# Kernel tuning notes

Measured on AMD Instinct MI355X. Metric: run time of the kernel, lower is better.

## Reference

```python
import jax, jax.numpy as jnp
import numpy as np

REPARAM_OFFSET = 2.0 ** -18
PEDESTAL = REPARAM_OFFSET ** 2            # 2**-36
BETA_MIN = 1e-6
BOUND_BETA = float(np.sqrt(BETA_MIN + PEDESTAL))
BOUND_A = float(np.sqrt(0.0 + PEDESTAL))


def nn_reparam(p, bound):
    # NonNegativeParametrizer.forward: lower_bound(p, bound)**2 - pedestal
    return jnp.maximum(p, bound) ** 2 - PEDESTAL


def setup_inputs() -> dict:
    key = jax.random.key(0)
    kx, ka = jax.random.split(key)
    C, R = 192, 8
    x = jax.random.normal(kx, (8, C, 256, 256), dtype=jnp.float32)
    # parameters stored in reparam-init space: init(v) = sqrt(max(v + ped, ped))
    beta = jnp.sqrt(jnp.ones((C,), jnp.float32) + PEDESTAL)
    A = jnp.sqrt(0.1 * jax.random.uniform(ka, (C, R), dtype=jnp.float32) + PEDESTAL)
    return {"x": x, "beta": beta, "A": A}


def reference(x, beta, A):
    beta_r = nn_reparam(beta, BOUND_BETA)[None, :, None, None]   # [1,C,1,1]
    A_r = nn_reparam(A, BOUND_A)                                  # [C,r]
    x2 = x * x
    T = jnp.einsum('nchw,cr->nrhw', x2, A_r)                      # low-rank projection
    denom_sq = jnp.einsum('cr,nrhw->nchw', A_r, T) + beta_r
    return x * jax.lax.rsqrt(denom_sq)                            # inverse=False -> rsqrt
```

## Files before the change

kernel.cpp:

```cpp
#include <hip/hip_runtime.h>


#define N_IMG 8
#define C_CH 192
#define R_RK 8
#define HW 65536
#define PXB 128
#define CSLICES 8
#define CPT (C_CH / CSLICES)
#define NTHR 512
#define BLOCKS_PER_IMG (HW / PXB)

#define PEDESTAL_F 1.4551915228366852e-11f
#define BOUND_A_F 3.814697265625e-06f
#define BOUND_BETA_F 1.0000072759311364e-03f

typedef float v2 __attribute__((ext_vector_type(2)));

__global__ __launch_bounds__(NTHR, 8) void lrgdn_kernel(
    const float* __restrict__ x,
    const float* __restrict__ beta,
    const float* __restrict__ A,
    float* __restrict__ out)
{
    __shared__ float sA[C_CH][R_RK];
    __shared__ float sB[C_CH];
    __shared__ v2 sT[CSLICES][R_RK][64];

    const int tid = threadIdx.x;

    for (int i = tid; i < C_CH * R_RK; i += NTHR) {
        float a = fmaxf(A[i], BOUND_A_F);
        sA[i >> 3][i & 7] = a * a - PEDESTAL_F;
    }
    if (tid < C_CH) {
        float b = fmaxf(beta[tid], BOUND_BETA_F);
        sB[tid] = b * b - PEDESTAL_F;
    }
    __syncthreads();

    const int blk  = blockIdx.x;
    const int n    = blk / BLOCKS_PER_IMG;
    const int p0   = (blk % BLOCKS_PER_IMG) * PXB;
    const int lane = tid & 63;
    const int cs   = tid >> 6;
    const int c0   = cs * CPT;

    const float* xn = x   + (size_t)n * (C_CH * HW) + p0 + (size_t)c0 * HW + 2 * lane;
    float*       on = out + (size_t)n * (C_CH * HW) + p0 + (size_t)c0 * HW + 2 * lane;

    v2 T[R_RK];
#pragma unroll
    for (int r = 0; r < R_RK; ++r) T[r] = (v2)0.f;

#pragma unroll 8
    for (int i = 0; i < CPT; ++i) {
        v2 v = *reinterpret_cast<const v2*>(xn + (size_t)i * HW);
        v2 s = v * v;
#pragma unroll
        for (int r = 0; r < R_RK; ++r) {
            T[r] += s * sA[c0 + i][r];
        }
    }

#pragma unroll
    for (int r = 0; r < R_RK; ++r) {
        sT[cs][r][lane] = T[r];
    }
    __syncthreads();

#pragma unroll
    for (int r = 0; r < R_RK; ++r) {
        v2 a01 = sT[0][r][lane] + sT[1][r][lane];
        v2 a23 = sT[2][r][lane] + sT[3][r][lane];
        v2 a45 = sT[4][r][lane] + sT[5][r][lane];
        v2 a67 = sT[6][r][lane] + sT[7][r][lane];
        T[r] = (a01 + a23) + (a45 + a67);
    }

#pragma unroll 8
    for (int i = 0; i < CPT; ++i) {
        int c = c0 + i;
        v2 v = *reinterpret_cast<const v2*>(xn + (size_t)i * HW);
        v2 d;
        d.x = sB[c];
        d.y = d.x;
#pragma unroll
        for (int r = 0; r < R_RK; ++r) {
            d += sA[c][r] * T[r];
        }
        v2 o;
        o.x = v.x * __builtin_amdgcn_rsqf(d.x);
        o.y = v.y * __builtin_amdgcn_rsqf(d.y);
        __builtin_nontemporal_store(o, reinterpret_cast<v2*>(on + (size_t)i * HW));
    }
}

extern "C" void kernel_launch(void* const* d_in, const int* in_sizes, int n_in,
                              void* d_out, int out_size, void* d_ws, size_t ws_size,
                              hipStream_t stream) {
    const float* x    = (const float*)d_in[0];
    const float* beta = (const float*)d_in[1];
    const float* A    = (const float*)d_in[2];
    float* out = (float*)d_out;

    dim3 grid(N_IMG * BLOCKS_PER_IMG);
    dim3 block(NTHR);
    hipLaunchKernelGGL(lrgdn_kernel, grid, block, 0, stream, x, beta, A, out);
}
```

Baseline: 206.2 us.

## Cache x in registers, halve pixel tile, and remap blocks across XCDs

Each thread now loads its 24 channel values once into registers with nontemporal loads and reuses them for the output pass, so the second global read of x goes away. The pixel tile drops from 128 to 64 with scalar per-thread access instead of float2, which doubles the grid. A block-index permutation spreads consecutive work across the 8 XCDs. The cost is more register pressure, narrower memory transactions and more blocks, each repeating the setup of the A and beta tables.

```diff
diff --git a/kernel.cpp b/kernel.cpp
--- a/kernel.cpp
+++ b/kernel.cpp
@@ -5,17 +5,16 @@
 #define C_CH 192
 #define R_RK 8
 #define HW 65536
-#define PXB 128
+#define PXB 64
 #define CSLICES 8
 #define CPT (C_CH / CSLICES)
 #define NTHR 512
 #define BLOCKS_PER_IMG (HW / PXB)
+#define NBLK (N_IMG * BLOCKS_PER_IMG)
 
 #define PEDESTAL_F 1.4551915228366852e-11f
 #define BOUND_A_F 3.814697265625e-06f
 #define BOUND_BETA_F 1.0000072759311364e-03f
-
-typedef float v2 __attribute__((ext_vector_type(2)));
 
 __global__ __launch_bounds__(NTHR, 8) void lrgdn_kernel(
     const float* __restrict__ x,
@@ -25,7 +24,7 @@
 {
     __shared__ float sA[C_CH][R_RK];
     __shared__ float sB[C_CH];
-    __shared__ v2 sT[CSLICES][R_RK][64];
+    __shared__ float sT[CSLICES][R_RK][64];
 
     const int tid = threadIdx.x;
 
@@ -39,27 +38,33 @@
     }
     __syncthreads();
 
-    const int blk  = blockIdx.x;
-    const int n    = blk / BLOCKS_PER_IMG;
-    const int p0   = (blk % BLOCKS_PER_IMG) * PXB;
+    const int b = blockIdx.x;
+    const int w = (b & 7) * (NBLK / 8) + (b >> 3);
+    const int n    = w / BLOCKS_PER_IMG;
+    const int p0   = (w % BLOCKS_PER_IMG) * PXB;
     const int lane = tid & 63;
     const int cs   = tid >> 6;
     const int c0   = cs * CPT;
 
-    const float* xn = x   + (size_t)n * (C_CH * HW) + p0 + (size_t)c0 * HW + 2 * lane;
-    float*       on = out + (size_t)n * (C_CH * HW) + p0 + (size_t)c0 * HW + 2 * lane;
+    const float* xn = x   + (size_t)n * (C_CH * HW) + p0 + (size_t)c0 * HW + lane;
+    float*       on = out + (size_t)n * (C_CH * HW) + p0 + (size_t)c0 * HW + lane;
 
-    v2 T[R_RK];
+    float xr[CPT];
 #pragma unroll
-    for (int r = 0; r < R_RK; ++r) T[r] = (v2)0.f;
+    for (int i = 0; i < CPT; ++i) {
+        xr[i] = __builtin_nontemporal_load(xn + (size_t)i * HW);
+    }
 
-#pragma unroll 8
+    float T[R_RK];
+#pragma unroll
+    for (int r = 0; r < R_RK; ++r) T[r] = 0.f;
+
+#pragma unroll
     for (int i = 0; i < CPT; ++i) {
-        v2 v = *reinterpret_cast<const v2*>(xn + (size_t)i * HW);
-        v2 s = v * v;
+        float s = xr[i] * xr[i];
 #pragma unroll
         for (int r = 0; r < R_RK; ++r) {
-            T[r] += s * sA[c0 + i][r];
+            T[r] = fmaf(s, sA[c0 + i][r], T[r]);
         }
     }
 
@@ -71,28 +76,23 @@
 
 #pragma unroll
     for (int r = 0; r < R_RK; ++r) {
-        v2 a01 = sT[0][r][lane] + sT[1][r][lane];
-        v2 a23 = sT[2][r][lane] + sT[3][r][lane];
-        v2 a45 = sT[4][r][lane] + sT[5][r][lane];
-        v2 a67 = sT[6][r][lane] + sT[7][r][lane];
+        float a01 = sT[0][r][lane] + sT[1][r][lane];
+        float a23 = sT[2][r][lane] + sT[3][r][lane];
+        float a45 = sT[4][r][lane] + sT[5][r][lane];
+        float a67 = sT[6][r][lane] + sT[7][r][lane];
         T[r] = (a01 + a23) + (a45 + a67);
     }
 
-#pragma unroll 8
+#pragma unroll
     for (int i = 0; i < CPT; ++i) {
         int c = c0 + i;
-        v2 v = *reinterpret_cast<const v2*>(xn + (size_t)i * HW);
-        v2 d;
-        d.x = sB[c];
-        d.y = d.x;
+        float d = sB[c];
 #pragma unroll
         for (int r = 0; r < R_RK; ++r) {
-            d += sA[c][r] * T[r];
+            d = fmaf(sA[c][r], T[r], d);
         }
-        v2 o;
-        o.x = v.x * __builtin_amdgcn_rsqf(d.x);
-        o.y = v.y * __builtin_amdgcn_rsqf(d.y);
-        __builtin_nontemporal_store(o, reinterpret_cast<v2*>(on + (size_t)i * HW));
+        float o = xr[i] * __builtin_amdgcn_rsqf(d);
+        __builtin_nontemporal_store(o, on + (size_t)i * HW);
     }
 }
 
@@ -104,7 +104,7 @@
     const float* A    = (const float*)d_in[2];
     float* out = (float*)d_out;
 
-    dim3 grid(N_IMG * BLOCKS_PER_IMG);
+    dim3 grid(NBLK);
     dim3 block(NTHR);
     hipLaunchKernelGGL(lrgdn_kernel, grid, block, 0, stream, x, beta, A, out);
 }
```

Measured after the change: 170.1 us. 1.21x faster.
